# Kernel tuning notes

Measured on AMD Instinct MI355X. Metric: run time of the kernel, lower is better.

## Reference

```python
import jax, jax.numpy as jnp
import numpy as np

INF = 1000000.0
B, S, D = 4, 1024, 768
NH, DH = 12, 64
LN_EPS = 1e-9


def _relative_shift_gather(pos_attn, context_len, shift):
    # pos_attn: [b, n, seq_len, max_rel_len]
    b, n, s, m = pos_attn.shape
    x = pos_attn.reshape(b, n, m, s)[:, :, shift:, :]
    x = x.reshape(b, n, s, m - shift)[..., :context_len]
    return x


def setup_inputs() -> dict:
    key = jax.random.key(0)
    ks = jax.random.split(key, 24)
    std = 0.02
    inp = {
        'query': jax.random.normal(ks[0], (B, S, D), jnp.float32),
        'key': jax.random.normal(ks[1], (B, S, D), jnp.float32),
        'value': jax.random.normal(ks[2], (B, S, D), jnp.float32),
        'r': jax.random.normal(ks[3], (2 * S - 1, D), jnp.float32),
        'token_type_mat': jax.random.randint(ks[4], (B, S, S), 0, 2) > 0,
        'attention_mask': jnp.ones((B, S), jnp.int32),
        'cls_mask': jnp.ones((1, 1, S, S), jnp.float32),
        'Wq': jax.random.normal(ks[5], (D, NH * DH), jnp.float32) * std,
        'Wk': jax.random.normal(ks[6], (D, NH * DH), jnp.float32) * std,
        'bk': jnp.zeros((NH * DH,), jnp.float32),
        'Wv': jax.random.normal(ks[7], (D, NH * DH), jnp.float32) * std,
        'bv': jnp.zeros((NH * DH,), jnp.float32),
        'Wpost': jax.random.normal(ks[8], (NH * DH, D), jnp.float32) * std,
        'bpost': jnp.zeros((D,), jnp.float32),
        'ln_g': jnp.ones((D,), jnp.float32),
        'ln_b': jnp.zeros((D,), jnp.float32),
        'r_w_bias': jax.random.normal(ks[9], (NH, DH), jnp.float32) * std,
        'r_r_bias': jax.random.normal(ks[10], (NH, DH), jnp.float32) * std,
        'r_kernel': jax.random.normal(ks[11], (D, NH, DH), jnp.float32) * std,
        'r_s_bias': jax.random.normal(ks[12], (NH, DH), jnp.float32) * std,
        'seg_embed': jax.random.normal(ks[13], (2, NH, DH), jnp.float32) * std,
    }
    return inp


def reference(query, key, value, r, token_type_mat, attention_mask, cls_mask,
              Wq, Wk, bk, Wv, bv, Wpost, bpost, ln_g, ln_b,
              r_w_bias, r_r_bias, r_kernel, r_s_bias, seg_embed):
    b, s, d_model = query.shape
    n_head, d_head = r_w_bias.shape
    context_len = key.shape[1]
    scale = 1.0 / d_head ** 0.5

    q_head = (query @ Wq).reshape(b, s, n_head, d_head) * scale   # bind
    k_head = (key @ Wk + bk).reshape(b, context_len, n_head, d_head)
    v_head = (value @ Wv + bv).reshape(b, context_len, n_head, d_head)

    # content score
    content_score = jnp.einsum('bind,bjnd->bnij', q_head + r_w_bias * scale, k_head)

    # relative positional attention (relative_shift path, shift=1 since s == context_len)
    shift = 2 if s != context_len else 1
    r_head = jnp.einsum('td,dnh->tnh', r, r_kernel)
    positional_attn = jnp.einsum('binh,tnh->bnit', q_head + r_r_bias * scale, r_head)
    positional_attn = _relative_shift_gather(positional_attn, context_len, shift)
    positional_attn = positional_attn * cls_mask

    # relative token-type (segment) attention
    token_type_bias = jnp.einsum('bind,snd->bnis', q_head + r_s_bias * scale, seg_embed)
    diff_tt = token_type_bias[..., 0:1]  # [b,n,i,1]
    same_tt = token_type_bias[..., 1:2]
    token_type_attn = jnp.where(token_type_mat[:, None], same_tt, diff_tt) * cls_mask

    attn_score = content_score + positional_attn + token_type_attn
    attn_score = attn_score - INF * (1.0 - attention_mask[:, None, None].astype(jnp.float32))
    attn_prob = jax.nn.softmax(attn_score, axis=-1)

    attn_vec = jnp.einsum('bnij,bjnd->bind', attn_prob, v_head)
    attn_out = attn_vec.reshape(b, s, n_head * d_head) @ Wpost + bpost

    x = query + attn_out
    mean = jnp.mean(x, axis=-1, keepdims=True)
    var = jnp.var(x, axis=-1, keepdims=True)
    out = (x - mean) * jax.lax.rsqrt(var + LN_EPS) * ln_g + ln_b
    return out
```

## Files before the change

### kernel.cpp

```cpp
#include <hip/hip_runtime.h>
#include <hip/hip_bf16.h>

#define S_LEN   1024
#define D_MODEL 768
#define N_HEAD  12
#define D_HEAD  64
#define BATCH   4
#define T_LEN   2047
#define INF_VAL 1000000.0f
#define SCALE   0.125f
#define LN_EPSF 1e-9f

typedef __attribute__((ext_vector_type(8))) __bf16 bf8;
typedef __attribute__((ext_vector_type(4))) __bf16 bf4;
typedef __attribute__((ext_vector_type(4))) float  f32x4;

__device__ __forceinline__ int swz_addr(int row, int byte_in_row) {
    return ((row << 7) + byte_in_row) ^ ((row & 7) << 4);
}

__global__ void detect_kernel(const unsigned char* __restrict__ p, int* __restrict__ flag)
{
    int lane = threadIdx.x;
    int nz = 0;
    int base = lane * 64;
    for (int k = base; k < base + 64; k += 4)
        nz += (p[k+1] != 0) + (p[k+2] != 0) + (p[k+3] != 0);
    unsigned long long m = __ballot(nz != 0);
    if (lane == 0) { flag[0] = (m == 0ull) ? 1 : 0; flag[1] = 1; }
}

__global__ __launch_bounds__(256)
void tobf16_kernel(const float* __restrict__ q, const float* __restrict__ k,
                   const float* __restrict__ v, const float* __restrict__ r,
                   __bf16* __restrict__ qb, __bf16* __restrict__ kb,
                   __bf16* __restrict__ vb, __bf16* __restrict__ rb)
{
    int z = blockIdx.z;
    const float* src; __bf16* dst; size_t n;
    if (z == 0)      { src = q; dst = qb; n = (size_t)4096*768; }
    else if (z == 1) { src = k; dst = kb; n = (size_t)4096*768; }
    else if (z == 2) { src = v; dst = vb; n = (size_t)4096*768; }
    else             { src = r; dst = rb; n = (size_t)T_LEN*768; }
    size_t i = ((size_t)blockIdx.x * 256 + threadIdx.x) * 8;
    if (i + 8 > n) return;
    float4 a = *(const float4*)(src + i);
    float4 b = *(const float4*)(src + i + 4);
    bf8 o;
    o[0]=(__bf16)a.x; o[1]=(__bf16)a.y; o[2]=(__bf16)a.z; o[3]=(__bf16)a.w;
    o[4]=(__bf16)b.x; o[5]=(__bf16)b.y; o[6]=(__bf16)b.z; o[7]=(__bf16)b.w;
    *(bf8*)(dst + i) = o;
}

__global__ __launch_bounds__(256)
void prep_sel(const void* __restrict__ ttm, const int* __restrict__ flag,
              unsigned char* __restrict__ selbit)
{
    size_t idx = ((size_t)blockIdx.x * 256 + threadIdx.x) * 8;
    unsigned long long out = 0;
    if (flag[0]) {
        const int* ip = (const int*)ttm + idx;
        int4 a = *(const int4*)ip;
        int4 b = *(const int4*)(ip + 4);
        out  = (a.x ? 1ull : 0)       | (a.y ? 1ull : 0) << 8
             | (a.z ? 1ull : 0) << 16 | (a.w ? 1ull : 0) << 24
             | (b.x ? 1ull : 0) << 32 | (b.y ? 1ull : 0) << 40
             | (b.z ? 1ull : 0) << 48 | (b.w ? 1ull : 0) << 56;
    } else {
        unsigned long long raw = *(const unsigned long long*)((const unsigned char*)ttm + idx);
        #pragma unroll
        for (int i = 0; i < 8; ++i)
            out |= (((raw >> (8*i)) & 0xffull) ? 1ull : 0) << (8*i);
    }
    *(unsigned long long*)(selbit + idx) = out;
}

__global__ __launch_bounds__(256)
void clsb_prep(const float* __restrict__ cls, const int* __restrict__ amask,
               __bf16* __restrict__ clsb, float* __restrict__ maskadd,
               int* __restrict__ flag)
{
    size_t idx = ((size_t)blockIdx.x * 256 + threadIdx.x) * 8;
    const float* p = cls + idx;
    float4 a = *(const float4*)p;
    float4 b = *(const float4*)(p + 4);
    bf8 o;
    o[0]=(__bf16)a.x; o[1]=(__bf16)a.y; o[2]=(__bf16)a.z; o[3]=(__bf16)a.w;
    o[4]=(__bf16)b.x; o[5]=(__bf16)b.y; o[6]=(__bf16)b.z; o[7]=(__bf16)b.w;
    *(bf8*)(clsb + idx) = o;
    int ok = (a.x==1.f)&&(a.y==1.f)&&(a.z==1.f)&&(a.w==1.f)
          && (b.x==1.f)&&(b.y==1.f)&&(b.z==1.f)&&(b.w==1.f);
    if (blockIdx.x == 0) {
        for (int j = threadIdx.x; j < BATCH * S_LEN; j += 256) {
            int am = amask[j];
            maskadd[j] = -INF_VAL * (1.f - (float)am);
            ok &= (am == 1);
        }
    }
    ok = __syncthreads_and(ok);
    if (threadIdx.x == 0 && !ok) atomicAnd(flag + 1, 0);
}

__global__ __launch_bounds__(256)
void wtrans_kernel(const float* __restrict__ W0, const float* __restrict__ W1,
                   const float* __restrict__ W2, const float* __restrict__ W3,
                   const float* __restrict__ W4,
                   __bf16* __restrict__ T0, __bf16* __restrict__ T1,
                   __bf16* __restrict__ T2, __bf16* __restrict__ T3,
                   __bf16* __restrict__ T4)
{
    const float* W; __bf16* Wt;
    switch (blockIdx.z) {
        case 0: W = W0; Wt = T0; break;
        case 1: W = W1; Wt = T1; break;
        case 2: W = W2; Wt = T2; break;
        case 3: W = W3; Wt = T3; break;
        default: W = W4; Wt = T4; break;
    }
    const int K = 768, N = 768;
    __shared__ float tile[64][65];
    int tid = threadIdx.x;
    int r = tid >> 4, c4 = (tid & 15) * 4;
    int k0 = blockIdx.y * 64, n0 = blockIdx.x * 64;
    #pragma unroll
    for (int rep = 0; rep < 4; ++rep) {
        int row = rep * 16 + r;
        float4 v = *(const float4*)(W + (size_t)(k0 + row) * N + n0 + c4);
        tile[row][c4+0] = v.x; tile[row][c4+1] = v.y;
        tile[row][c4+2] = v.z; tile[row][c4+3] = v.w;
    }
    __syncthreads();
    #pragma unroll
    for (int rep = 0; rep < 4; ++rep) {
        int row = rep * 16 + r;
        bf4 o;
        #pragma unroll
        for (int j = 0; j < 4; ++j) o[j] = (__bf16)tile[c4 + j][row];
        *(bf4*)(Wt + (size_t)(n0 + row) * K + k0 + c4) = o;
    }
}

__device__ __forceinline__
void gemm_tile_body(const __bf16* __restrict__ A, const __bf16* __restrict__ Bt,
                    const float* __restrict__ bias, void* __restrict__ C,
                    int M, int N, int K, float scale, int has_bias,
                    int out_mode, int m0, int n0, __bf16* As, __bf16* Bs)
{
    int tid = threadIdx.x;
    int lane = tid & 63, w = tid >> 6;
    int grp = lane >> 4, lcol = lane & 15;
    int wm = w >> 1, wn = w & 1;

    auto loadA = [&](int kt, int rep) -> bf8 {
        int id = rep * 256 + tid;
        int row = id >> 3, ch = id & 7;
        int gm = m0 + row; if (gm >= M) gm = M - 1;
        return *(const bf8*)(A + (size_t)gm * K + kt + ch * 8);
    };
    auto loadB = [&](int kt, int rep) -> bf8 {
        int id = rep * 256 + tid;
        int row = id >> 3, ch = id & 7;
        return *(const bf8*)(Bt + (size_t)(n0 + row) * K + kt + ch * 8);
    };

    bf8 aR0 = loadA(0,0), aR1 = loadA(0,1), aR2 = loadA(0,2), aR3 = loadA(0,3);
    bf8 bR0 = loadB(0,0), bR1 = loadB(0,1), bR2 = loadB(0,2), bR3 = loadB(0,3);

    f32x4 acc[4][4] = {};

    for (int kt = 0; kt < K; kt += 64) {
        __syncthreads();
        {
            int id0 = tid;
            { int id = 0*256 + id0; int row = id >> 3, ch = id & 7;
              *(bf8*)((char*)As + swz_addr(row, ch*16)) = aR0;
              *(bf8*)((char*)Bs + swz_addr(row, ch*16)) = bR0; }
            { int id = 1*256 + id0; int row = id >> 3, ch = id & 7;
              *(bf8*)((char*)As + swz_addr(row, ch*16)) = aR1;
              *(bf8*)((char*)Bs + swz_addr(row, ch*16)) = bR1; }
            { int id = 2*256 + id0; int row = id >> 3, ch = id & 7;
              *(bf8*)((char*)As + swz_addr(row, ch*16)) = aR2;
              *(bf8*)((char*)Bs + swz_addr(row, ch*16)) = bR2; }
            { int id = 3*256 + id0; int row = id >> 3, ch = id & 7;
              *(bf8*)((char*)As + swz_addr(row, ch*16)) = aR3;
              *(bf8*)((char*)Bs + swz_addr(row, ch*16)) = bR3; }
        }
        __syncthreads();
        if (kt + 64 < K) {
            aR0 = loadA(kt+64,0); aR1 = loadA(kt+64,1); aR2 = loadA(kt+64,2); aR3 = loadA(kt+64,3);
            bR0 = loadB(kt+64,0); bR1 = loadB(kt+64,1); bR2 = loadB(kt+64,2); bR3 = loadB(kt+64,3);
        }
        #pragma unroll
        for (int kk = 0; kk < 2; ++kk) {
            bf8 a[4], bb[4];
            #pragma unroll
            for (int mi = 0; mi < 4; ++mi)
                a[mi] = *(const bf8*)((const char*)As + swz_addr(wm * 64 + mi * 16 + lcol, kk * 64 + grp * 16));
            #pragma unroll
            for (int ni = 0; ni < 4; ++ni)
                bb[ni] = *(const bf8*)((const char*)Bs + swz_addr(wn * 64 + ni * 16 + lcol, kk * 64 + grp * 16));
            #pragma unroll
            for (int mi = 0; mi < 4; ++mi) {
                #pragma unroll
                for (int ni = 0; ni < 4; ++ni)
                    acc[mi][ni] = __builtin_amdgcn_mfma_f32_16x16x32_bf16(a[mi], bb[ni], acc[mi][ni], 0, 0, 0);
            }
        }
    }

    #pragma unroll
    for (int ni = 0; ni < 4; ++ni) {
        int col = n0 + wn * 64 + ni * 16 + lcol;
        float bval = has_bias ? bias[col] : 0.f;
        #pragma unroll
        for (int mi = 0; mi < 4; ++mi) {
            int rbase = m0 + wm * 64 + mi * 16 + grp * 4;
            if (out_mode == 2) {
                int hn = col >> 6, d = col & 63;
                int bb2 = rbase >> 10;
                int j = rbase & 1023;
                bf4 o;
                #pragma unroll
                for (int reg = 0; reg < 4; ++reg)
                    o[reg] = (__bf16)(acc[mi][ni][reg] * scale + bval);
                *(bf4*)((__bf16*)C + ((size_t)(bb2 * N_HEAD + hn) * 64 + d) * 1024 + j) = o;
            } else {
                #pragma unroll
                for (int reg = 0; reg < 4; ++reg) {
                    int row = rbase + reg;
                    if (row < M) {
                        float vv = acc[mi][ni][reg] * scale + bval;
                        if (out_mode == 1) ((__bf16*)C)[(size_t)row * N + col] = (__bf16)vv;
                        else               ((float*)C)[(size_t)row * N + col] = vv;
                    }
                }
            }
        }
    }
}

__global__ __launch_bounds__(256, 3)
void proj_gemm(const __bf16* __restrict__ qb, const __bf16* __restrict__ kb,
               const __bf16* __restrict__ vb, const __bf16* __restrict__ rb,
               const __bf16* __restrict__ Wqt, const __bf16* __restrict__ Wkt,
               const __bf16* __restrict__ Wvt, const __bf16* __restrict__ rkt,
               const float* __restrict__ bk, const float* __restrict__ bv,
               __bf16* __restrict__ qh, __bf16* __restrict__ kh,
               __bf16* __restrict__ vhT, __bf16* __restrict__ rhd)
{
    __shared__ __align__(16) __bf16 As[128 * 64];
    __shared__ __align__(16) __bf16 Bs[128 * 64];
    int id = blockIdx.x;
    int wg = (id & 7) * 96 + (id >> 3);
    int z  = wg / 192;
    int rem = wg % 192;
    int by = rem / 6, bx = rem % 6;

    const __bf16* A; const __bf16* Bt; const float* bias; void* C;
    int M; float scale; int has_bias; int omode;
    if (z == 0)      { A = qb; Bt = Wqt; bias = nullptr; C = qh;  M = 4096; scale = SCALE; has_bias = 0; omode = 1; }
    else if (z == 1) { A = kb; Bt = Wkt; bias = bk;      C = kh;  M = 4096; scale = 1.f;   has_bias = 1; omode = 1; }
    else if (z == 2) { A = vb; Bt = Wvt; bias = bv;      C = vhT; M = 4096; scale = 1.f;   has_bias = 1; omode = 2; }
    else             { A = rb; Bt = rkt; bias = nullptr; C = rhd; M = T_LEN; scale = 1.f;  has_bias = 0; omode = 1; }
    int m0 = by * 128, n0 = bx * 128;
    if (m0 >= M) return;
    gemm_tile_body(A, Bt, bias, C, M, 768, 768, scale, has_bias, omode, m0, n0, As, Bs);
}

__global__ __launch_bounds__(256, 3)
void post_gemm(const __bf16* __restrict__ av, const __bf16* __restrict__ Wpt,
               const float* __restrict__ bpost, float* __restrict__ ao)
{
    __shared__ __align__(16) __bf16 As[128 * 64];
    __shared__ __align__(16) __bf16 Bs[128 * 64];
    int id = blockIdx.x;
    int wg = (id & 7) * 24 + (id >> 3);
    int by = wg / 6, bx = wg % 6;
    gemm_tile_body(av, Wpt, bpost, ao, 4096, 768, 768, 1.f, 1, 0,
                   by * 128, bx * 128, As, Bs);
}

__global__ __launch_bounds__(256)
void ttbias_kernel(const __bf16* __restrict__ qh, const float* __restrict__ rsb,
                   const float* __restrict__ seg, float* __restrict__ tt)
{
    int idx = blockIdx.x * 256 + threadIdx.x;
    if (idx >= BATCH * S_LEN * N_HEAD * 2) return;
    int s2  = idx & 1;
    int n   = (idx >> 1) % N_HEAD;
    int row = idx / (2 * N_HEAD);
    const __bf16* q  = qh  + (size_t)row * D_MODEL + n * D_HEAD;
    const float* sg = seg + ((size_t)s2 * N_HEAD + n) * D_HEAD;
    const float* rb = rsb + n * D_HEAD;
    float s = 0.f;
    for (int h = 0; h < D_HEAD; ++h) s += ((float)q[h] + rb[h] * SCALE) * sg[h];
    tt[idx] = s;
}

__global__ __launch_bounds__(256, 3)
void attn_kernel(const __bf16* __restrict__ qh, const __bf16* __restrict__ kh,
                 const __bf16* __restrict__ vhT, const __bf16* __restrict__ rhd,
                 const float* __restrict__ tt, const __bf16* __restrict__ clsb,
                 const unsigned char* __restrict__ selbit,
                 const float* __restrict__ maskadd,
                 const float* __restrict__ rwb, const float* __restrict__ rrb,
                 const int* __restrict__ flag, __bf16* __restrict__ av)
{
    __shared__ __align__(16) __bf16 Kt[64*64];
    __shared__ __align__(16) __bf16 Vt[64*64];
    __shared__ __align__(16) __bf16 Rw[128*64];
    __shared__ __align__(16) __bf16 Ps[4*16*64];
    __shared__ __align__(16) __bf16 poss[4*16*84];

    int tid = threadIdx.x;
    int i0 = blockIdx.x * 64;
    int n  = blockIdx.y;
    int b  = blockIdx.z;
    int bS = b * S_LEN;
    int n64 = n * D_HEAD;
    int simple = flag[1];

    int lane = tid & 63, w = tid >> 6;
    int grp = lane >> 4, lcol = lane & 15;

    const __bf16* vT = vhT + (size_t)(b * N_HEAD + n) * 64 * 1024;

    bf8 qwA[2], qrA[2];
    {
        size_t qrow = (size_t)(bS + i0 + w*16 + lcol) * D_MODEL + n64;
        #pragma unroll
        for (int kk = 0; kk < 2; ++kk) {
            int kb = kk*32 + grp*8;
            bf8 qv = *(const bf8*)(qh + qrow + kb);
            const float* wbp = rwb + n64 + kb;
            const float* rbp = rrb + n64 + kb;
            #pragma unroll
            for (int q = 0; q < 8; ++q) {
                float f = (float)qv[q];
                qwA[kk][q] = (__bf16)(f + wbp[q] * SCALE);
                qrA[kk][q] = (__bf16)(f + rbp[q] * SCALE);
            }
        }
    }

    float t0r[4], t1r[4];
    #pragma unroll
    for (int reg = 0; reg < 4; ++reg) {
        int gi = i0 + w*16 + grp*4 + reg;
        const float* ttrow = tt + (((size_t)(bS + gi)) * N_HEAD + n) * 2;
        t0r[reg] = ttrow[0];
        t1r[reg] = ttrow[1];
    }

    float fixv = 0.f;
    if (i0 == 0) {
        float qv = (float)qh[((size_t)(bS + 1)) * D_MODEL + n64 + lane] + rrb[n64 + lane] * SCALE;
        float rv = (float)rhd[n64 + lane];
        float t = qv * rv;
        #pragma unroll
        for (int m = 32; m; m >>= 1) t += __shfl_xor(t, m, 64);
        fixv = t;
    }
    bool fix = (i0 == 0 && w == 0 && lane == 15);

    float m_run[4] = {-1e30f, -1e30f, -1e30f, -1e30f};
    float l_run[4] = {0.f, 0.f, 0.f, 0.f};
    f32x4 acc[4] = {};
    const f32x4 zero4 = {0.f, 0.f, 0.f, 0.f};

    for (int jt = 0; jt < 16; ++jt) {
        int j0 = jt * 64;
        int w0 = j0 - i0 + 961;
        __syncthreads();

        #pragma unroll
        for (int rep = 0; rep < 2; ++rep) {
            int idx = rep*256 + tid;
            int row = idx >> 3;
            int c8  = (idx & 7) * 8;
            bf8 v = *(const bf8*)(kh + (size_t)(bS + j0 + row) * D_MODEL + n64 + c8);
            *(bf8*)((char*)Kt + swz_addr(row, c8*2)) = v;
        }
        #pragma unroll
        for (int rep = 0; rep < 2; ++rep) {
            int idx = rep*256 + tid;
            int row = idx >> 3;
            int jc  = (idx & 7) * 8;
            bf8 v = *(const bf8*)(vT + (size_t)row * 1024 + j0 + jc);
            *(bf8*)((char*)Vt + swz_addr(row, jc*2)) = v;
        }
        if (jt == 0) {
            #pragma unroll
            for (int rep = 0; rep < 4; ++rep) {
                int idx = rep*256 + tid;
                int rowl = idx >> 3;
                int c8  = (idx & 7) * 8;
                int t = w0 + rowl;
                bf8 v = {};
                if (t < T_LEN)
                    v = *(const bf8*)(rhd + (size_t)t * D_MODEL + n64 + c8);
                *(bf8*)((char*)Rw + swz_addr(t & 127, c8*2)) = v;
            }
        } else {
            #pragma unroll
            for (int rep = 0; rep < 2; ++rep) {
                int idx = rep*256 + tid;
                int rowl = idx >> 3;
                int c8  = (idx & 7) * 8;
                int t = w0 + 64 + rowl;
                bf8 v = {};
                if (t < T_LEN)
                    v = *(const bf8*)(rhd + (size_t)t * D_MODEL + n64 + c8);
                *(bf8*)((char*)Rw + swz_addr(t & 127, c8*2)) = v;
            }
        }
        __syncthreads();

        f32x4 sc_[4] = {zero4, zero4, zero4, zero4};
        #pragma unroll
        for (int c = 0; c < 4; ++c) {
            #pragma unroll
            for (int kk = 0; kk < 2; ++kk) {
                bf8 kb2 = *(const bf8*)((const char*)Kt + swz_addr(c*16 + lcol, kk*64 + grp*16));
                sc_[c] = __builtin_amdgcn_mfma_f32_16x16x32_bf16(qwA[kk], kb2, sc_[c], 0, 0, 0);
            }
        }
        int a0 = 3 - w;
        f32x4 pacc[5] = {zero4, zero4, zero4, zero4, zero4};
        #pragma unroll
        for (int pa = 0; pa < 5; ++pa) {
            #pragma unroll
            for (int kk = 0; kk < 2; ++kk) {
                int tr = w0 + (a0 + pa) * 16 + lcol;
                bf8 rb2 = *(const bf8*)((const char*)Rw + swz_addr(tr & 127, kk*64 + grp*16));
                pacc[pa] = __builtin_amdgcn_mfma_f32_16x16x32_bf16(qrA[kk], rb2, pacc[pa], 0, 0, 0);
            }
        }
        __bf16* pw = poss + w * 16 * 84;
        #pragma unroll
        for (int pa = 0; pa < 5; ++pa) {
            #pragma unroll
            for (int reg = 0; reg < 4; ++reg)
                pw[(grp*4 + reg) * 84 + pa*16 + lcol] = (__bf16)pacc[pa][reg];
        }
        asm volatile("s_waitcnt lgkmcnt(0)" ::: "memory");
        __builtin_amdgcn_sched_barrier(0);

        float sv[4][4];
        if (simple) {
            #pragma unroll
            for (int c = 0; c < 4; ++c) {
                int jl = c*16 + lcol;
                int gj = j0 + jl;
                #pragma unroll
                for (int reg = 0; reg < 4; ++reg) {
                    int il = grp*4 + reg;
                    int gi = i0 + w*16 + il;
                    int rr = jl - il + 15;
                    float pv = (float)pw[il * 84 + rr];
                    if (fix && jt == 15 && c == 3 && reg == 0) pv = fixv;
                    float ttv = selbit[((size_t)(bS + gi)) * S_LEN + gj] ? t1r[reg] : t0r[reg];
                    sv[c][reg] = sc_[c][reg] + pv + ttv;
                }
            }
        } else {
            #pragma unroll
            for (int c = 0; c < 4; ++c) {
                int jl = c*16 + lcol;
                int gj = j0 + jl;
                float ma = maskadd[b * S_LEN + gj];
                #pragma unroll
                for (int reg = 0; reg < 4; ++reg) {
                    int il = grp*4 + reg;
                    int gi = i0 + w*16 + il;
                    int rr = jl - il + 15;
                    float pv = (float)pw[il * 84 + rr];
                    if (fix && jt == 15 && c == 3 && reg == 0) pv = fixv;
                    float clv = (float)clsb[(size_t)gi * S_LEN + gj];
                    float ttv = selbit[((size_t)(bS + gi)) * S_LEN + gj] ? t1r[reg] : t0r[reg];
                    sv[c][reg] = sc_[c][reg] + clv * (pv + ttv) + ma;
                }
            }
        }

        float mx[4], alpha[4], rs[4];
        #pragma unroll
        for (int reg = 0; reg < 4; ++reg)
            mx[reg] = fmaxf(fmaxf(sv[0][reg], sv[1][reg]), fmaxf(sv[2][reg], sv[3][reg]));
        #pragma unroll
        for (int msk = 1; msk < 16; msk <<= 1) {
            #pragma unroll
            for (int reg = 0; reg < 4; ++reg)
                mx[reg] = fmaxf(mx[reg], __shfl_xor(mx[reg], msk, 64));
        }
        #pragma unroll
        for (int reg = 0; reg < 4; ++reg) {
            float mn = fmaxf(m_run[reg], mx[reg]);
            alpha[reg] = __expf(m_run[reg] - mn);
            m_run[reg] = mn;
            rs[reg] = 0.f;
        }
        __bf16* psw = Ps;
        #pragma unroll
        for (int c = 0; c < 4; ++c) {
            int jl = c*16 + lcol;
            #pragma unroll
            for (int reg = 0; reg < 4; ++reg) {
                int il = grp*4 + reg;
                float p = __expf(sv[c][reg] - m_run[reg]);
                rs[reg] += p;
                *((__bf16*)((char*)psw + w*2048 + swz_addr(il, jl*2))) = (__bf16)p;
            }
        }
        #pragma unroll
        for (int msk = 1; msk < 16; msk <<= 1) {
            #pragma unroll
            for (int reg = 0; reg < 4; ++reg)
                rs[reg] += __shfl_xor(rs[reg], msk, 64);
        }
        #pragma unroll
        for (int reg = 0; reg < 4; ++reg)
            l_run[reg] = l_run[reg] * alpha[reg] + rs[reg];
        #pragma unroll
        for (int c = 0; c < 4; ++c) {
            #pragma unroll
            for (int reg = 0; reg < 4; ++reg) acc[c][reg] *= alpha[reg];
        }
        asm volatile("s_waitcnt lgkmcnt(0)" ::: "memory");
        __builtin_amdgcn_sched_barrier(0);

        bf8 pA[2];
        #pragma unroll
        for (int kk = 0; kk < 2; ++kk)
            pA[kk] = *(const bf8*)((const char*)psw + w*2048 + swz_addr(lcol, kk*64 + grp*16));
        #pragma unroll
        for (int c = 0; c < 4; ++c) {
            #pragma unroll
            for (int kk = 0; kk < 2; ++kk) {
                bf8 vb2 = *(const bf8*)((const char*)Vt + swz_addr(c*16 + lcol, kk*64 + grp*16));
                acc[c] = __builtin_amdgcn_mfma_f32_16x16x32_bf16(pA[kk], vb2, acc[c], 0, 0, 0);
            }
        }
    }

    float inv[4];
    #pragma unroll
    for (int reg = 0; reg < 4; ++reg) inv[reg] = 1.f / l_run[reg];
    #pragma unroll
    for (int c = 0; c < 4; ++c) {
        #pragma unroll
        for (int reg = 0; reg < 4; ++reg) {
            size_t o = ((size_t)(bS + i0 + w*16 + grp*4 + reg)) * D_MODEL + n64 + c*16 + lcol;
            av[o] = (__bf16)(acc[c][reg] * inv[reg]);
        }
    }
}

__global__ __launch_bounds__(256)
void ln_kernel(const float* __restrict__ query, const float* __restrict__ ao,
               const float* __restrict__ gam, const float* __restrict__ bet,
               float* __restrict__ out)
{
    int row = blockIdx.x;
    int tid = threadIdx.x;
    size_t base = (size_t)row * D_MODEL;
    float xv[3];
    float s = 0.f, sq = 0.f;
    #pragma unroll
    for (int k = 0; k < 3; ++k) {
        int c = tid + k * 256;
        float v = query[base + c] + ao[base + c];
        xv[k] = v; s += v; sq += v * v;
    }
    for (int off = 32; off > 0; off >>= 1) {
        s  += __shfl_down(s, off);
        sq += __shfl_down(sq, off);
    }
    __shared__ float rs[4], rq[4];
    __shared__ float mean_s, inv_s;
    int wid = tid >> 6, lane = tid & 63;
    if (lane == 0) { rs[wid] = s; rq[wid] = sq; }
    __syncthreads();
    if (tid == 0) {
        float S0 = rs[0] + rs[1] + rs[2] + rs[3];
        float Q0 = rq[0] + rq[1] + rq[2] + rq[3];
        float mean = S0 / (float)D_MODEL;
        float var  = Q0 / (float)D_MODEL - mean * mean;
        mean_s = mean;
        inv_s  = rsqrtf(var + LN_EPSF);
    }
    __syncthreads();
    float mean = mean_s, inv = inv_s;
    #pragma unroll
    for (int k = 0; k < 3; ++k) {
        int c = tid + k * 256;
        out[base + c] = (xv[k] - mean) * inv * gam[c] + bet[c];
    }
}

extern "C" void kernel_launch(void* const* d_in, const int* in_sizes, int n_in,
                              void* d_out, int out_size, void* d_ws, size_t ws_size,
                              hipStream_t stream)
{
    const float* query = (const float*)d_in[0];
    const float* key   = (const float*)d_in[1];
    const float* value = (const float*)d_in[2];
    const float* r     = (const float*)d_in[3];
    const void*  ttm   = d_in[4];
    const int*   amask = (const int*)d_in[5];
    const float* cls   = (const float*)d_in[6];
    const float* Wq    = (const float*)d_in[7];
    const float* Wk    = (const float*)d_in[8];
    const float* bk    = (const float*)d_in[9];
    const float* Wv    = (const float*)d_in[10];
    const float* bv    = (const float*)d_in[11];
    const float* Wpost = (const float*)d_in[12];
    const float* bpost = (const float*)d_in[13];
    const float* ln_g  = (const float*)d_in[14];
    const float* ln_b  = (const float*)d_in[15];
    const float* rwb   = (const float*)d_in[16];
    const float* rrb   = (const float*)d_in[17];
    const float* rker  = (const float*)d_in[18];
    const float* rsb   = (const float*)d_in[19];
    const float* seg   = (const float*)d_in[20];

    char* wsb = (char*)d_ws;
    __bf16* qh  = (__bf16*)(wsb);
    __bf16* kh  = (__bf16*)(wsb + 6291456);
    __bf16* vhT = (__bf16*)(wsb + 12582912);
    __bf16* rhd = (__bf16*)(wsb + 18874368);
    float*  tt  = (float*) (wsb + 22020096);
    __bf16* av  = (__bf16*)(wsb + 22413312);
    float*  ao  = (float*) (wsb + 28704768);
    __bf16* Wqt = (__bf16*)(wsb + 41287680);
    __bf16* Wkt = (__bf16*)(wsb + 42467328);
    __bf16* Wvt = (__bf16*)(wsb + 43646976);
    __bf16* Wpt = (__bf16*)(wsb + 44826624);
    __bf16* rkt = (__bf16*)(wsb + 46006272);
    int*    flag = (int*)  (wsb + 47185920);
    unsigned char* selbit = (unsigned char*)(wsb + 47186176);
    __bf16* clsb    = (__bf16*)(wsb + 51380480);
    float*  maskadd = (float*) (wsb + 53477632);
    __bf16* rin_b   = (__bf16*)(wsb + 53494016);

    __bf16* qin_b = av;
    __bf16* kin_b = (__bf16*)ao;
    __bf16* vin_b = (__bf16*)(wsb + 34996224);

    detect_kernel<<<1, 64, 0, stream>>>((const unsigned char*)ttm, flag);
    tobf16_kernel<<<dim3(1536, 1, 4), 256, 0, stream>>>(query, key, value, r,
                                                        qin_b, kin_b, vin_b, rin_b);
    prep_sel<<<2048, 256, 0, stream>>>(ttm, flag, selbit);
    clsb_prep<<<512, 256, 0, stream>>>(cls, amask, clsb, maskadd, flag);

    dim3 gtr(12, 12, 5);
    wtrans_kernel<<<gtr, 256, 0, stream>>>(Wq, Wk, Wv, Wpost, rker,
                                           Wqt, Wkt, Wvt, Wpt, rkt);

    proj_gemm<<<768, 256, 0, stream>>>(qin_b, kin_b, vin_b, rin_b,
                                       Wqt, Wkt, Wvt, rkt, bk, bv,
                                       qh, kh, vhT, rhd);

    ttbias_kernel<<<384, 256, 0, stream>>>(qh, rsb, seg, tt);

    dim3 gattn(16, 12, 4);
    attn_kernel<<<gattn, 256, 0, stream>>>(qh, kh, vhT, rhd, tt, clsb, selbit,
                                           maskadd, rwb, rrb, flag, av);

    post_gemm<<<192, 256, 0, stream>>>(av, Wpt, bpost, ao);

    ln_kernel<<<4096, 256, 0, stream>>>(query, ao, ln_g, ln_b, (float*)d_out);
}
```

Measured before the change: 173.9 us.

## Bit-pack token-type selector and replace LDS relative-shift staging with lane shuffles

The token-type selector is now packed into one bit per element (64 columns per 64-bit word) instead of one byte per element. The attention kernel loads a single word per row per key tile rather than a byte per score. The positional scores are also no longer staged through a shared-memory buffer for the diagonal relative shift. Each lane now fetches the shifted values from neighbouring lanes with cross-lane shuffles and picks between adjacent MFMA tiles, which removes the LDS writes, a waitcnt and the 'poss' buffer. The cost is 20 shuffles per tile and extra register pressure, and the index mapping must be exactly right.

```diff
diff --git a/kernel.cpp b/kernel.cpp
--- a/kernel.cpp
+++ b/kernel.cpp
@@ -54,25 +54,31 @@
 
 __global__ __launch_bounds__(256)
 void prep_sel(const void* __restrict__ ttm, const int* __restrict__ flag,
-              unsigned char* __restrict__ selbit)
-{
-    size_t idx = ((size_t)blockIdx.x * 256 + threadIdx.x) * 8;
+              unsigned long long* __restrict__ selpack)
+{
+    size_t widx = (size_t)blockIdx.x * 256 + threadIdx.x;
     unsigned long long out = 0;
     if (flag[0]) {
-        const int* ip = (const int*)ttm + idx;
-        int4 a = *(const int4*)ip;
-        int4 b = *(const int4*)(ip + 4);
-        out  = (a.x ? 1ull : 0)       | (a.y ? 1ull : 0) << 8
-             | (a.z ? 1ull : 0) << 16 | (a.w ? 1ull : 0) << 24
-             | (b.x ? 1ull : 0) << 32 | (b.y ? 1ull : 0) << 40
-             | (b.z ? 1ull : 0) << 48 | (b.w ? 1ull : 0) << 56;
+        const int* ip = (const int*)ttm + widx * 64;
+        #pragma unroll
+        for (int g = 0; g < 16; ++g) {
+            int4 a = *(const int4*)(ip + g * 4);
+            unsigned long long nib = (a.x ? 1u : 0u) | (a.y ? 2u : 0u)
+                                   | (a.z ? 4u : 0u) | (a.w ? 8u : 0u);
+            out |= nib << (g * 4);
+        }
     } else {
-        unsigned long long raw = *(const unsigned long long*)((const unsigned char*)ttm + idx);
-        #pragma unroll
-        for (int i = 0; i < 8; ++i)
-            out |= (((raw >> (8*i)) & 0xffull) ? 1ull : 0) << (8*i);
-    }
-    *(unsigned long long*)(selbit + idx) = out;
+        const unsigned long long* p8 =
+            (const unsigned long long*)((const unsigned char*)ttm + widx * 64);
+        #pragma unroll
+        for (int g = 0; g < 8; ++g) {
+            unsigned long long raw = p8[g];
+            #pragma unroll
+            for (int k = 0; k < 8; ++k)
+                if ((raw >> (8*k)) & 0xffull) out |= 1ull << (g*8 + k);
+        }
+    }
+    selpack[widx] = out;
 }
 
 __global__ __launch_bounds__(256)
@@ -301,7 +307,7 @@
 void attn_kernel(const __bf16* __restrict__ qh, const __bf16* __restrict__ kh,
                  const __bf16* __restrict__ vhT, const __bf16* __restrict__ rhd,
                  const float* __restrict__ tt, const __bf16* __restrict__ clsb,
-                 const unsigned char* __restrict__ selbit,
+                 const unsigned long long* __restrict__ selpack,
                  const float* __restrict__ maskadd,
                  const float* __restrict__ rwb, const float* __restrict__ rrb,
                  const int* __restrict__ flag, __bf16* __restrict__ av)
@@ -310,7 +316,6 @@
     __shared__ __align__(16) __bf16 Vt[64*64];
     __shared__ __align__(16) __bf16 Rw[128*64];
     __shared__ __align__(16) __bf16 Ps[4*16*64];
-    __shared__ __align__(16) __bf16 poss[4*16*84];
 
     int tid = threadIdx.x;
     int i0 = blockIdx.x * 64;
@@ -352,6 +357,13 @@
         t1r[reg] = ttrow[1];
     }
 
+    int srcl[4];
+    #pragma unroll
+    for (int reg = 0; reg < 4; ++reg) {
+        int il = grp*4 + reg;
+        srcl[reg] = (grp << 4) | ((lcol + 15 - il) & 15);
+    }
+
     float fixv = 0.f;
     if (i0 == 0) {
         float qv = (float)qh[((size_t)(bS + 1)) * D_MODEL + n64 + lane] + rrb[n64 + lane] * SCALE;
@@ -372,6 +384,13 @@
         int j0 = jt * 64;
         int w0 = j0 - i0 + 961;
         __syncthreads();
+
+        unsigned long long selw[4];
+        #pragma unroll
+        for (int reg = 0; reg < 4; ++reg) {
+            int gi = i0 + w*16 + grp*4 + reg;
+            selw[reg] = selpack[(size_t)(bS + gi) * 16 + jt];
+        }
 
         #pragma unroll
         for (int rep = 0; rep < 2; ++rep) {
@@ -436,30 +455,26 @@
                 pacc[pa] = __builtin_amdgcn_mfma_f32_16x16x32_bf16(qrA[kk], rb2, pacc[pa], 0, 0, 0);
             }
         }
-        __bf16* pw = poss + w * 16 * 84;
-        #pragma unroll
-        for (int pa = 0; pa < 5; ++pa) {
-            #pragma unroll
-            for (int reg = 0; reg < 4; ++reg)
-                pw[(grp*4 + reg) * 84 + pa*16 + lcol] = (__bf16)pacc[pa][reg];
-        }
-        asm volatile("s_waitcnt lgkmcnt(0)" ::: "memory");
-        __builtin_amdgcn_sched_barrier(0);
+
+        float sp[4][5];
+        #pragma unroll
+        for (int reg = 0; reg < 4; ++reg) {
+            #pragma unroll
+            for (int pa = 0; pa < 5; ++pa)
+                sp[reg][pa] = __shfl(pacc[pa][reg], srcl[reg], 64);
+        }
 
         float sv[4][4];
         if (simple) {
             #pragma unroll
             for (int c = 0; c < 4; ++c) {
                 int jl = c*16 + lcol;
-                int gj = j0 + jl;
                 #pragma unroll
                 for (int reg = 0; reg < 4; ++reg) {
                     int il = grp*4 + reg;
-                    int gi = i0 + w*16 + il;
-                    int rr = jl - il + 15;
-                    float pv = (float)pw[il * 84 + rr];
+                    float pv = (lcol > il) ? sp[reg][c+1] : sp[reg][c];
                     if (fix && jt == 15 && c == 3 && reg == 0) pv = fixv;
-                    float ttv = selbit[((size_t)(bS + gi)) * S_LEN + gj] ? t1r[reg] : t0r[reg];
+                    float ttv = ((selw[reg] >> jl) & 1ull) ? t1r[reg] : t0r[reg];
                     sv[c][reg] = sc_[c][reg] + pv + ttv;
                 }
             }
@@ -473,11 +488,10 @@
                 for (int reg = 0; reg < 4; ++reg) {
                     int il = grp*4 + reg;
                     int gi = i0 + w*16 + il;
-                    int rr = jl - il + 15;
-                    float pv = (float)pw[il * 84 + rr];
+                    float pv = (lcol > il) ? sp[reg][c+1] : sp[reg][c];
                     if (fix && jt == 15 && c == 3 && reg == 0) pv = fixv;
                     float clv = (float)clsb[(size_t)gi * S_LEN + gj];
-                    float ttv = selbit[((size_t)(bS + gi)) * S_LEN + gj] ? t1r[reg] : t0r[reg];
+                    float ttv = ((selw[reg] >> jl) & 1ull) ? t1r[reg] : t0r[reg];
                     sv[c][reg] = sc_[c][reg] + clv * (pv + ttv) + ma;
                 }
             }
@@ -638,7 +652,7 @@
     __bf16* Wpt = (__bf16*)(wsb + 44826624);
     __bf16* rkt = (__bf16*)(wsb + 46006272);
     int*    flag = (int*)  (wsb + 47185920);
-    unsigned char* selbit = (unsigned char*)(wsb + 47186176);
+    unsigned long long* selpack = (unsigned long long*)(wsb + 47186176);
     __bf16* clsb    = (__bf16*)(wsb + 51380480);
     float*  maskadd = (float*) (wsb + 53477632);
     __bf16* rin_b   = (__bf16*)(wsb + 53494016);
@@ -650,7 +664,7 @@
     detect_kernel<<<1, 64, 0, stream>>>((const unsigned char*)ttm, flag);
     tobf16_kernel<<<dim3(1536, 1, 4), 256, 0, stream>>>(query, key, value, r,
                                                         qin_b, kin_b, vin_b, rin_b);
-    prep_sel<<<2048, 256, 0, stream>>>(ttm, flag, selbit);
+    prep_sel<<<256, 256, 0, stream>>>(ttm, flag, selpack);
     clsb_prep<<<512, 256, 0, stream>>>(cls, amask, clsb, maskadd, flag);
 
     dim3 gtr(12, 12, 5);
@@ -664,7 +678,7 @@
     ttbias_kernel<<<384, 256, 0, stream>>>(qh, rsb, seg, tt);
 
     dim3 gattn(16, 12, 4);
-    attn_kernel<<<gattn, 256, 0, stream>>>(qh, kh, vhT, rhd, tt, clsb, selbit,
+    attn_kernel<<<gattn, 256, 0, stream>>>(qh, kh, vhT, rhd, tt, clsb, selpack,
                                            maskadd, rwb, rrb, flag, av);
 
     post_gemm<<<192, 256, 0, stream>>>(av, Wpt, bpost, ao);
```

Result: slower. 222.7 us (+28.1%).
